# Kernel tuning notes

Measured on AMD Instinct MI355X. Metric: run time of the kernel, lower is better.

The kernel has to match this reference:

```python
import jax, jax.numpy as jnp
import numpy as np

ALPHA = 0.2  # LeakyReLU negative slope
OUT_FEATURES = 64

def setup_inputs() -> dict:
    key = jax.random.key(0)
    k1, k2, k3 = jax.random.split(key, 3)
    B, N, F_in, F_out = 16, 2048, 64, OUT_FEATURES
    h = jax.random.normal(k1, (B, N, F_in), dtype=jnp.float32)
    W = jax.random.normal(k2, (F_in, F_out), dtype=jnp.float32) * (1.414 / np.sqrt(F_in))
    a = jax.random.normal(k3, (2 * F_out, 1), dtype=jnp.float32) * 1.414
    return {"h": h, "W": W, "a": a}

def reference(h, W, a):
    F_out = W.shape[1]
    Wh = jnp.matmul(h, W)                        # [B, N, F_out]
    Wh1 = jnp.matmul(Wh, a[:F_out, :])           # [B, N, 1]
    Wh2 = jnp.matmul(Wh, a[F_out:, :])           # [B, N, 1]
    e = Wh1 + jnp.transpose(Wh2, (0, 2, 1))      # [B, N, N] broadcast add
    e = jnp.where(e >= 0, e, ALPHA * e)          # LeakyReLU
    attention = jax.nn.softmax(jax.nn.sigmoid(e), axis=1)  # softmax over dim=1 (faithful to source)
    h_prime = jnp.matmul(attention, Wh)          # [B, N, F_out]
    return jax.nn.elu(h_prime)                   # concat=True -> ELU
```

## Files before the change

### kernel.cpp

```cpp
#include <hip/hip_runtime.h>
#include <hip/hip_bf16.h>
#include <math.h>

#define NB 16
#define NN 2048
#define NF 64
#define LOG2E 1.44269504f

#define NT 4096
#define T_LO (-40.0f)
#define T_HI (10.0f)
#define T_SCALE (NT / (T_HI - T_LO))
#define Z_BIAS (-T_LO * T_SCALE)
#define Z_MAX ((float)(NT - 1))

#define MG 512
#define XG_LO (-96.0f)
#define DXG 0.375f
#define INV_DXG (1.0f / DXG)
#define U_BIAS (-XG_LO * INV_DXG)
#define U_MAX 510.999f

typedef __attribute__((ext_vector_type(8))) __bf16 bf16x8;
typedef __attribute__((ext_vector_type(8))) short  short8;
typedef __attribute__((ext_vector_type(4))) float  f32x4;

__device__ __forceinline__ float gexact(float t) {
    float v = t >= 0.f ? t : 0.2f * t;
    float s = 1.f / (1.f + expf(-v));
    return expf(s);
}

__device__ __forceinline__ float tlookup(const float* __restrict__ stab, float z) {
    float zc = __builtin_amdgcn_fmed3f(z, 0.f, Z_MAX);
    return stab[(int)zc];
}

__device__ __forceinline__ float elu(float v) {
    return v > 0.f ? v : (__builtin_amdgcn_exp2f(v * LOG2E) - 1.f);
}

__global__ __launch_bounds__(256) void k_prep(const float* __restrict__ h,
                                              const float* __restrict__ W,
                                              const float* __restrict__ a,
                                              uint4* __restrict__ vfrag,
                                              float* __restrict__ xs,
                                              float* __restrict__ ys,
                                              float* __restrict__ xs_u,
                                              float* __restrict__ ys_u,
                                              float* __restrict__ gtab) {
    __shared__ __attribute__((aligned(16))) float  hT[64 * 68];
    __shared__ __attribute__((aligned(16))) __bf16 WbT[64 * 72];
    __shared__ __attribute__((aligned(16))) __bf16 vT[64 * 74];
    __shared__ float uv[128];
    int t  = threadIdx.x;
    int r0 = blockIdx.x * 64;
    int b  = blockIdx.x >> 5;
    const float4* hsrc = (const float4*)(h + r0 * 64);
#pragma unroll
    for (int i = 0; i < 4; i++) {
        int flat = t + i * 256;
        int row = flat >> 4, c4 = flat & 15;
        float4 hv = hsrc[flat];
        float* dst = &hT[row * 68 + c4 * 4];
        dst[0] = hv.x; dst[1] = hv.y; dst[2] = hv.z; dst[3] = hv.w;
    }
#pragma unroll
    for (int i = 0; i < 4; i++) {
        int flat = t + i * 256;
        int k = flat >> 4, c4 = flat & 15;
        float4 wv = ((const float4*)W)[flat];
        WbT[(c4 * 4 + 0) * 72 + k] = (__bf16)wv.x;
        WbT[(c4 * 4 + 1) * 72 + k] = (__bf16)wv.y;
        WbT[(c4 * 4 + 2) * 72 + k] = (__bf16)wv.z;
        WbT[(c4 * 4 + 3) * 72 + k] = (__bf16)wv.w;
    }
    if (t < 64) {
        float s = 0.f;
#pragma unroll 8
        for (int f = 0; f < 64; f++) s = fmaf(W[t * 64 + f], a[f], s);
        uv[t] = s;
    } else if (t < 128) {
        int k = t - 64;
        float s = 0.f;
#pragma unroll 8
        for (int f = 0; f < 64; f++) s = fmaf(W[k * 64 + f], a[64 + f], s);
        uv[64 + k] = s;
    }
    __syncthreads();
    {
        int row = t >> 2, q = t & 3;
        const float* hp = &hT[row * 68 + q * 16];
        const float* up = &uv[q * 16];
        const float* vp = &uv[64 + q * 16];
        float sx = 0.f, sy = 0.f;
#pragma unroll
        for (int k2 = 0; k2 < 16; k2++) {
            float hv = hp[k2];
            sx = fmaf(hv, up[k2], sx);
            sy = fmaf(hv, vp[k2], sy);
        }
        sx += __shfl_xor(sx, 1); sx += __shfl_xor(sx, 2);
        sy += __shfl_xor(sy, 1); sy += __shfl_xor(sy, 2);
        if (q == 0) {
            int r = r0 + row;
            xs[r]   = T_SCALE * sx;
            ys[r]   = T_SCALE * sy;
            xs_u[r] = __builtin_amdgcn_fmed3f(sx * INV_DXG + U_BIAS, 0.f, U_MAX);
            ys_u[r] = __builtin_amdgcn_fmed3f(sy * INV_DXG + U_BIAS, 0.f, U_MAX);
        }
    }
    int w = t >> 6, lane = t & 63;
    int il = lane & 15, kg = lane >> 4;
    f32x4 acc0 = {0.f,0.f,0.f,0.f}, acc1 = {0.f,0.f,0.f,0.f};
    f32x4 acc2 = {0.f,0.f,0.f,0.f}, acc3 = {0.f,0.f,0.f,0.f};
#pragma unroll
    for (int ks = 0; ks < 2; ks++) {
        const float* ap = &hT[(w * 16 + il) * 68 + ks * 32 + kg * 8];
        bf16x8 af;
#pragma unroll
        for (int e = 0; e < 8; e++) af[e] = (__bf16)ap[e];
        bf16x8 b0 = *(const bf16x8*)&WbT[(0 * 16 + il) * 72 + ks * 32 + kg * 8];
        bf16x8 b1 = *(const bf16x8*)&WbT[(1 * 16 + il) * 72 + ks * 32 + kg * 8];
        bf16x8 b2 = *(const bf16x8*)&WbT[(2 * 16 + il) * 72 + ks * 32 + kg * 8];
        bf16x8 b3 = *(const bf16x8*)&WbT[(3 * 16 + il) * 72 + ks * 32 + kg * 8];
        acc0 = __builtin_amdgcn_mfma_f32_16x16x32_bf16(af, b0, acc0, 0, 0, 0);
        acc1 = __builtin_amdgcn_mfma_f32_16x16x32_bf16(af, b1, acc1, 0, 0, 0);
        acc2 = __builtin_amdgcn_mfma_f32_16x16x32_bf16(af, b2, acc2, 0, 0, 0);
        acc3 = __builtin_amdgcn_mfma_f32_16x16x32_bf16(af, b3, acc3, 0, 0, 0);
    }
#pragma unroll
    for (int r = 0; r < 4; r++) {
        __bf16* vrow = &vT[(w * 16 + kg * 4 + r) * 74 + il];
        vrow[0]  = (__bf16)acc0[r];
        vrow[16] = (__bf16)acc1[r];
        vrow[32] = (__bf16)acc2[r];
        vrow[48] = (__bf16)acc3[r];
    }
    __syncthreads();
#pragma unroll
    for (int s = 0; s < 2; s++) {
        int oi    = t + s * 256;
        int lane2 = oi & 63;
        int nt2   = (oi >> 6) & 3;
        int ksl   = oi >> 8;
        int rbase = ksl * 32 + ((lane2 >> 4) << 3);
        int col   = nt2 * 16 + (lane2 & 15);
        short8 o;
#pragma unroll
        for (int e = 0; e < 8; e++)
            o[e] = __builtin_bit_cast(short, vT[(rbase + e) * 74 + col]);
        int ks_g = ((blockIdx.x & 31) << 1) | ksl;
        vfrag[((b * 64 + ks_g) * 4 + nt2) * 64 + lane2] = __builtin_bit_cast(uint4, o);
    }
    if (blockIdx.x < 16) {
        int i = blockIdx.x * 256 + t;
        gtab[i] = gexact(T_LO + ((float)i + 0.5f) / T_SCALE);
    }
}

__global__ __launch_bounds__(256) void k_fbuild(const float* __restrict__ xs,
                                                const float* __restrict__ gtab,
                                                float* __restrict__ F) {
    __shared__ float stab[NT];
    __shared__ float xsb[NN];
    int tid = threadIdx.x;
    {
        const float4* src = (const float4*)gtab;
        float4*       dst = (float4*)stab;
#pragma unroll
        for (int k = 0; k < NT / 4 / 256; k++) dst[tid + k * 256] = src[tid + k * 256];
    }
    int mg = blockIdx.x & 127;
    int b  = blockIdx.x >> 7;
    {
        const float4* src = (const float4*)(xs + b * NN);
        float4*       dst = (float4*)xsb;
#pragma unroll
        for (int k = 0; k < NN / 4 / 256; k++) dst[tid + k * 256] = src[tid + k * 256];
    }
    __syncthreads();
    int w = tid >> 6, lane = tid & 63;
    int m = mg * 4 + w;
    float ymb = (XG_LO + (float)m * DXG) * T_SCALE + Z_BIAS;
    float acc = 0.f;
#pragma unroll 8
    for (int i8 = 0; i8 < NN / 64; i8++)
        acc += tlookup(stab, xsb[i8 * 64 + lane] + ymb);
#pragma unroll
    for (int s = 32; s; s >>= 1) acc += __shfl_xor(acc, s, 64);
    if (lane == 0) F[b * MG + m] = acc;
}

__global__ __launch_bounds__(512) void k_gbuild(const float* __restrict__ ys,
                                                const float* __restrict__ ys_u,
                                                const float* __restrict__ F,
                                                const float* __restrict__ gtab,
                                                const uint4* __restrict__ vfrag,
                                                float* __restrict__ G) {
    __shared__ float stab[NT];
    __shared__ float dinvb[NN];
    __shared__ float red[7][16][65];
    {
        const float4* src = (const float4*)gtab;
        float4*       dst = (float4*)stab;
#pragma unroll
        for (int k = 0; k < NT / 4 / 512; k++) dst[threadIdx.x + k * 512] = src[threadIdx.x + k * 512];
    }
    int b  = blockIdx.x >> 5;
    int ib = blockIdx.x & 31;
    {
        const float* Fb = F + b * MG;
#pragma unroll
        for (int i = 0; i < 4; i++) {
            int j = threadIdx.x + i * 512;
            float u  = ys_u[b * NN + j];
            int   k  = (int)u;
            float fr = u - (float)k;
            float d  = fmaf(Fb[k + 1] - Fb[k], fr, Fb[k]);
            dinvb[j] = __builtin_amdgcn_rcpf(d);
        }
    }
    int kz = threadIdx.x >> 6, lane = threadIdx.x & 63;
    int il = lane & 15, kg = lane >> 4;
    int mbase = ib * 16;

    float xgb = (XG_LO + (float)(mbase + il) * DXG) * T_SCALE + Z_BIAS;
    const float* ysb = ys + b * NN;
    const uint4* vfb = vfrag + b * 16384 + lane;
    __syncthreads();

    f32x4 acc0 = {0.f,0.f,0.f,0.f}, acc1 = {0.f,0.f,0.f,0.f};
    f32x4 acc2 = {0.f,0.f,0.f,0.f}, acc3 = {0.f,0.f,0.f,0.f};

    for (int ks = kz * 8; ks < kz * 8 + 8; ks++) {
        const float* yp = ysb + ks * 32 + kg * 8;
        const float* dp = &dinvb[ks * 32 + kg * 8];
        float4 ya = *reinterpret_cast<const float4*>(yp);
        float4 yb = *reinterpret_cast<const float4*>(yp + 4);
        float wv[8];
        wv[0] = tlookup(stab, xgb + ya.x);
        wv[1] = tlookup(stab, xgb + ya.y);
        wv[2] = tlookup(stab, xgb + ya.z);
        wv[3] = tlookup(stab, xgb + ya.w);
        wv[4] = tlookup(stab, xgb + yb.x);
        wv[5] = tlookup(stab, xgb + yb.y);
        wv[6] = tlookup(stab, xgb + yb.z);
        wv[7] = tlookup(stab, xgb + yb.w);
        bf16x8 af;
#pragma unroll
        for (int e = 0; e < 8; e++) af[e] = (__bf16)(wv[e] * dp[e]);

        const uint4* vp = vfb + ks * 256;
        bf16x8 b0 = __builtin_bit_cast(bf16x8, vp[0]);
        bf16x8 b1 = __builtin_bit_cast(bf16x8, vp[64]);
        bf16x8 b2 = __builtin_bit_cast(bf16x8, vp[128]);
        bf16x8 b3 = __builtin_bit_cast(bf16x8, vp[192]);

        acc0 = __builtin_amdgcn_mfma_f32_16x16x32_bf16(af, b0, acc0, 0, 0, 0);
        acc1 = __builtin_amdgcn_mfma_f32_16x16x32_bf16(af, b1, acc1, 0, 0, 0);
        acc2 = __builtin_amdgcn_mfma_f32_16x16x32_bf16(af, b2, acc2, 0, 0, 0);
        acc3 = __builtin_amdgcn_mfma_f32_16x16x32_bf16(af, b3, acc3, 0, 0, 0);
    }

    if (kz > 0) {
#pragma unroll
        for (int r = 0; r < 4; r++) {
            float* rp = &red[kz - 1][kg * 4 + r][il];
            rp[0]  = acc0[r];
            rp[16] = acc1[r];
            rp[32] = acc2[r];
            rp[48] = acc3[r];
        }
    }
    __syncthreads();
    if (kz == 0) {
        int gbase = (b * MG + mbase + kg * 4) * 64 + il;
#pragma unroll
        for (int r = 0; r < 4; r++) {
            float s0 = acc0[r], s1 = acc1[r], s2 = acc2[r], s3 = acc3[r];
#pragma unroll
            for (int p = 0; p < 7; p++) {
                const float* rp = &red[p][kg * 4 + r][il];
                s0 += rp[0]; s1 += rp[16]; s2 += rp[32]; s3 += rp[48];
            }
            float* grow = G + gbase + r * 64;
            grow[0] = s0; grow[16] = s1; grow[32] = s2; grow[48] = s3;
        }
    }
}

__global__ __launch_bounds__(256) void k_apply(const float* __restrict__ xs_u,
                                               const float* __restrict__ G,
                                               float* __restrict__ out) {
    int w = threadIdx.x >> 6, f = threadIdx.x & 63;
    int r = blockIdx.x * 4 + w;
    int b = r >> 11;
    float u  = xs_u[r];
    int   k  = (int)u;
    float fr = u - (float)k;
    const float* Gb = G + (b * MG + k) * 64;
    float g0 = Gb[f];
    float g1 = Gb[64 + f];
    out[r * 64 + f] = elu(fmaf(g1 - g0, fr, g0));
}

extern "C" void kernel_launch(void* const* d_in, const int* in_sizes, int n_in,
                              void* d_out, int out_size, void* d_ws, size_t ws_size,
                              hipStream_t stream) {
    const float* h = (const float*)d_in[0];
    const float* W = (const float*)d_in[1];
    const float* a = (const float*)d_in[2];
    float* out = (float*)d_out;

    float*  xs    = (float*)d_ws;
    float*  ys    = xs + NB * NN;
    float*  xs_u  = ys + NB * NN;
    float*  ys_u  = xs_u + NB * NN;
    float*  F     = ys_u + NB * NN;
    float*  G     = F + NB * MG;
    uint4*  vfrag = (uint4*)(G + NB * MG * NF);
    float*  gtab  = (float*)(vfrag + NB * NN * NF / 8);

    k_prep<<<dim3(NB * NN / 64), dim3(256), 0, stream>>>(h, W, a, vfrag, xs, ys, xs_u, ys_u, gtab);
    k_fbuild<<<dim3(NB * (MG / 4)), dim3(256), 0, stream>>>(xs, gtab, F);
    k_gbuild<<<dim3(NB * (MG / 16)), dim3(512), 0, stream>>>(ys, ys_u, F, gtab, vfrag, G);
    k_apply<<<dim3(NB * NN / 4), dim3(256), 0, stream>>>(xs_u, G, out);
}
```

Measured before the change: 37.54 us.

## Replace F-build kernel with histogram convolution fused into G-build

Removes the separate k_fbuild launch, which did a table lookup for every x per grid point. Inside k_gbuild, each block now builds a linearly interpolated histogram of the batch's x values over the grid using LDS atomics. It then convolves that histogram with a precomputed 1D g table written by k_prep to get the column sums F. This cuts one launch and the O(N·M) lookups, but every gbuild block redundantly recomputes F (512x512 FMAs plus atomics) and adds interpolation error from binning x.

```diff
diff --git a/kernel.cpp b/kernel.cpp
--- a/kernel.cpp
+++ b/kernel.cpp
@@ -20,6 +20,7 @@
 #define INV_DXG (1.0f / DXG)
 #define U_BIAS (-XG_LO * INV_DXG)
 #define U_MAX 510.999f
+#define GS_N 1024
 
 typedef __attribute__((ext_vector_type(8))) __bf16 bf16x8;
 typedef __attribute__((ext_vector_type(8))) short  short8;
@@ -44,11 +45,11 @@
                                               const float* __restrict__ W,
                                               const float* __restrict__ a,
                                               uint4* __restrict__ vfrag,
-                                              float* __restrict__ xs,
                                               float* __restrict__ ys,
                                               float* __restrict__ xs_u,
                                               float* __restrict__ ys_u,
-                                              float* __restrict__ gtab) {
+                                              float* __restrict__ gtab,
+                                              float* __restrict__ gs) {
     __shared__ __attribute__((aligned(16))) float  hT[64 * 68];
     __shared__ __attribute__((aligned(16))) __bf16 WbT[64 * 72];
     __shared__ __attribute__((aligned(16))) __bf16 vT[64 * 74];
@@ -104,7 +105,6 @@
         sy += __shfl_xor(sy, 1); sy += __shfl_xor(sy, 2);
         if (q == 0) {
             int r = r0 + row;
-            xs[r]   = T_SCALE * sx;
             ys[r]   = T_SCALE * sy;
             xs_u[r] = __builtin_amdgcn_fmed3f(sx * INV_DXG + U_BIAS, 0.f, U_MAX);
             ys_u[r] = __builtin_amdgcn_fmed3f(sy * INV_DXG + U_BIAS, 0.f, U_MAX);
@@ -156,72 +156,62 @@
     if (blockIdx.x < 16) {
         int i = blockIdx.x * 256 + t;
         gtab[i] = gexact(T_LO + ((float)i + 0.5f) / T_SCALE);
-    }
-}
-
-__global__ __launch_bounds__(256) void k_fbuild(const float* __restrict__ xs,
-                                                const float* __restrict__ gtab,
-                                                float* __restrict__ F) {
-    __shared__ float stab[NT];
-    __shared__ float xsb[NN];
-    int tid = threadIdx.x;
-    {
-        const float4* src = (const float4*)gtab;
-        float4*       dst = (float4*)stab;
-#pragma unroll
-        for (int k = 0; k < NT / 4 / 256; k++) dst[tid + k * 256] = src[tid + k * 256];
-    }
-    int mg = blockIdx.x & 127;
-    int b  = blockIdx.x >> 7;
-    {
-        const float4* src = (const float4*)(xs + b * NN);
-        float4*       dst = (float4*)xsb;
-#pragma unroll
-        for (int k = 0; k < NN / 4 / 256; k++) dst[tid + k * 256] = src[tid + k * 256];
-    }
-    __syncthreads();
-    int w = tid >> 6, lane = tid & 63;
-    int m = mg * 4 + w;
-    float ymb = (XG_LO + (float)m * DXG) * T_SCALE + Z_BIAS;
-    float acc = 0.f;
-#pragma unroll 8
-    for (int i8 = 0; i8 < NN / 64; i8++)
-        acc += tlookup(stab, xsb[i8 * 64 + lane] + ymb);
-#pragma unroll
-    for (int s = 32; s; s >>= 1) acc += __shfl_xor(acc, s, 64);
-    if (lane == 0) F[b * MG + m] = acc;
+    } else if (blockIdx.x < 20) {
+        int i = (blockIdx.x - 16) * 256 + t;
+        gs[i] = gexact(2.f * XG_LO + (float)i * DXG);
+    }
 }
 
 __global__ __launch_bounds__(512) void k_gbuild(const float* __restrict__ ys,
                                                 const float* __restrict__ ys_u,
-                                                const float* __restrict__ F,
+                                                const float* __restrict__ xs_u,
                                                 const float* __restrict__ gtab,
+                                                const float* __restrict__ gs,
                                                 const uint4* __restrict__ vfrag,
                                                 float* __restrict__ G) {
     __shared__ float stab[NT];
     __shared__ float dinvb[NN];
     __shared__ float red[7][16][65];
+    float* gsb = &red[0][0][0];
+    float* hxb = gsb + GS_N;
+    float* Fb  = hxb + MG;
+    int t = threadIdx.x;
+    int b  = blockIdx.x >> 5;
+    int ib = blockIdx.x & 31;
     {
         const float4* src = (const float4*)gtab;
         float4*       dst = (float4*)stab;
 #pragma unroll
-        for (int k = 0; k < NT / 4 / 512; k++) dst[threadIdx.x + k * 512] = src[threadIdx.x + k * 512];
-    }
-    int b  = blockIdx.x >> 5;
-    int ib = blockIdx.x & 31;
+        for (int k = 0; k < NT / 4 / 512; k++) dst[t + k * 512] = src[t + k * 512];
+    }
+    if (t < 256) ((float4*)gsb)[t] = ((const float4*)gs)[t];
+    hxb[t] = 0.f;
+    __syncthreads();
+#pragma unroll
+    for (int i = 0; i < 4; i++) {
+        float xu = xs_u[b * NN + i * 512 + t];
+        int   k  = (int)xu;
+        float fr = xu - (float)k;
+        atomicAdd(&hxb[k],     1.f - fr);
+        atomicAdd(&hxb[k + 1], fr);
+    }
+    __syncthreads();
     {
-        const float* Fb = F + b * MG;
-#pragma unroll
-        for (int i = 0; i < 4; i++) {
-            int j = threadIdx.x + i * 512;
-            float u  = ys_u[b * NN + j];
-            int   k  = (int)u;
-            float fr = u - (float)k;
-            float d  = fmaf(Fb[k + 1] - Fb[k], fr, Fb[k]);
-            dinvb[j] = __builtin_amdgcn_rcpf(d);
-        }
-    }
-    int kz = threadIdx.x >> 6, lane = threadIdx.x & 63;
+        float acc = 0.f;
+        for (int k = 0; k < MG; k++) acc = fmaf(hxb[k], gsb[k + t], acc);
+        Fb[t] = acc;
+    }
+    __syncthreads();
+#pragma unroll
+    for (int i = 0; i < 4; i++) {
+        int j = t + i * 512;
+        float u  = ys_u[b * NN + j];
+        int   k  = (int)u;
+        float fr = u - (float)k;
+        float d  = fmaf(Fb[k + 1] - Fb[k], fr, Fb[k]);
+        dinvb[j] = __builtin_amdgcn_rcpf(d);
+    }
+    int kz = t >> 6, lane = t & 63;
     int il = lane & 15, kg = lane >> 4;
     int mbase = ib * 16;
 
@@ -313,17 +303,15 @@
     const float* a = (const float*)d_in[2];
     float* out = (float*)d_out;
 
-    float*  xs    = (float*)d_ws;
-    float*  ys    = xs + NB * NN;
+    float*  ys    = (float*)d_ws;
     float*  xs_u  = ys + NB * NN;
     float*  ys_u  = xs_u + NB * NN;
-    float*  F     = ys_u + NB * NN;
-    float*  G     = F + NB * MG;
+    float*  G     = ys_u + NB * NN;
     uint4*  vfrag = (uint4*)(G + NB * MG * NF);
     float*  gtab  = (float*)(vfrag + NB * NN * NF / 8);
-
-    k_prep<<<dim3(NB * NN / 64), dim3(256), 0, stream>>>(h, W, a, vfrag, xs, ys, xs_u, ys_u, gtab);
-    k_fbuild<<<dim3(NB * (MG / 4)), dim3(256), 0, stream>>>(xs, gtab, F);
-    k_gbuild<<<dim3(NB * (MG / 16)), dim3(512), 0, stream>>>(ys, ys_u, F, gtab, vfrag, G);
+    float*  gs    = gtab + NT;
+
+    k_prep<<<dim3(NB * NN / 64), dim3(256), 0, stream>>>(h, W, a, vfrag, ys, xs_u, ys_u, gtab, gs);
+    k_gbuild<<<dim3(NB * (MG / 16)), dim3(512), 0, stream>>>(ys, ys_u, xs_u, gtab, gs, vfrag, G);
     k_apply<<<dim3(NB * NN / 4), dim3(256), 0, stream>>>(xs_u, G, out);
 }
```

New measurement: 50.54 us. 1.35x slower.

## Fuse F-table build into prep kernel using grid-sampled g and atomics

Applied to the files above, without the earlier changes.

Drops the separate k_fbuild kernel. Each k_prep block now builds a small shared table of the exact g function on the DXG grid and uses its rows' grid-interpolated xs coordinates to add into F with atomicAdd. F is zeroed with a memset beforehand. This removes one kernel launch and the xs round trip through memory, but it changes the approximation: F is now built from interpolated grid values instead of the fine lookup table. It also adds per-block exp work, shared-memory reads and global atomics.

```diff
diff --git a/kernel.cpp b/kernel.cpp
--- a/kernel.cpp
+++ b/kernel.cpp
@@ -20,6 +20,7 @@
 #define INV_DXG (1.0f / DXG)
 #define U_BIAS (-XG_LO * INV_DXG)
 #define U_MAX 510.999f
+#define GS_N 1024
 
 typedef __attribute__((ext_vector_type(8))) __bf16 bf16x8;
 typedef __attribute__((ext_vector_type(8))) short  short8;
@@ -44,18 +45,24 @@
                                               const float* __restrict__ W,
                                               const float* __restrict__ a,
                                               uint4* __restrict__ vfrag,
-                                              float* __restrict__ xs,
                                               float* __restrict__ ys,
                                               float* __restrict__ xs_u,
                                               float* __restrict__ ys_u,
+                                              float* __restrict__ F,
                                               float* __restrict__ gtab) {
     __shared__ __attribute__((aligned(16))) float  hT[64 * 68];
     __shared__ __attribute__((aligned(16))) __bf16 WbT[64 * 72];
     __shared__ __attribute__((aligned(16))) __bf16 vT[64 * 74];
     __shared__ float uv[128];
+    __shared__ float gsb[GS_N];
+    __shared__ int   kuA[64];
+    __shared__ float frA[64];
     int t  = threadIdx.x;
     int r0 = blockIdx.x * 64;
     int b  = blockIdx.x >> 5;
+#pragma unroll
+    for (int i = t; i < GS_N; i += 256)
+        gsb[i] = gexact(2.f * XG_LO + (float)i * DXG);
     const float4* hsrc = (const float4*)(h + r0 * 64);
 #pragma unroll
     for (int i = 0; i < 4; i++) {
@@ -104,10 +111,13 @@
         sy += __shfl_xor(sy, 1); sy += __shfl_xor(sy, 2);
         if (q == 0) {
             int r = r0 + row;
-            xs[r]   = T_SCALE * sx;
+            float xu = __builtin_amdgcn_fmed3f(sx * INV_DXG + U_BIAS, 0.f, U_MAX);
             ys[r]   = T_SCALE * sy;
-            xs_u[r] = __builtin_amdgcn_fmed3f(sx * INV_DXG + U_BIAS, 0.f, U_MAX);
+            xs_u[r] = xu;
             ys_u[r] = __builtin_amdgcn_fmed3f(sy * INV_DXG + U_BIAS, 0.f, U_MAX);
+            int ku  = (int)xu;
+            kuA[row] = ku;
+            frA[row] = xu - (float)ku;
         }
     }
     int w = t >> 6, lane = t & 63;
@@ -153,43 +163,25 @@
         int ks_g = ((blockIdx.x & 31) << 1) | ksl;
         vfrag[((b * 64 + ks_g) * 4 + nt2) * 64 + lane2] = __builtin_bit_cast(uint4, o);
     }
+    {
+        float a0 = 0.f, a1 = 0.f;
+#pragma unroll 8
+        for (int r = 0; r < 64; r++) {
+            int   ku = kuA[r];
+            float fr = frA[r];
+            float w0 = 1.f - fr;
+            const float* g0 = &gsb[ku + t];
+            const float* g1 = &gsb[ku + t + 256];
+            a0 = fmaf(w0, g0[0], a0); a0 = fmaf(fr, g0[1], a0);
+            a1 = fmaf(w0, g1[0], a1); a1 = fmaf(fr, g1[1], a1);
+        }
+        atomicAdd(&F[b * MG + t], a0);
+        atomicAdd(&F[b * MG + t + 256], a1);
+    }
     if (blockIdx.x < 16) {
         int i = blockIdx.x * 256 + t;
         gtab[i] = gexact(T_LO + ((float)i + 0.5f) / T_SCALE);
     }
-}
-
-__global__ __launch_bounds__(256) void k_fbuild(const float* __restrict__ xs,
-                                                const float* __restrict__ gtab,
-                                                float* __restrict__ F) {
-    __shared__ float stab[NT];
-    __shared__ float xsb[NN];
-    int tid = threadIdx.x;
-    {
-        const float4* src = (const float4*)gtab;
-        float4*       dst = (float4*)stab;
-#pragma unroll
-        for (int k = 0; k < NT / 4 / 256; k++) dst[tid + k * 256] = src[tid + k * 256];
-    }
-    int mg = blockIdx.x & 127;
-    int b  = blockIdx.x >> 7;
-    {
-        const float4* src = (const float4*)(xs + b * NN);
-        float4*       dst = (float4*)xsb;
-#pragma unroll
-        for (int k = 0; k < NN / 4 / 256; k++) dst[tid + k * 256] = src[tid + k * 256];
-    }
-    __syncthreads();
-    int w = tid >> 6, lane = tid & 63;
-    int m = mg * 4 + w;
-    float ymb = (XG_LO + (float)m * DXG) * T_SCALE + Z_BIAS;
-    float acc = 0.f;
-#pragma unroll 8
-    for (int i8 = 0; i8 < NN / 64; i8++)
-        acc += tlookup(stab, xsb[i8 * 64 + lane] + ymb);
-#pragma unroll
-    for (int s = 32; s; s >>= 1) acc += __shfl_xor(acc, s, 64);
-    if (lane == 0) F[b * MG + m] = acc;
 }
 
 __global__ __launch_bounds__(512) void k_gbuild(const float* __restrict__ ys,
@@ -313,8 +305,7 @@
     const float* a = (const float*)d_in[2];
     float* out = (float*)d_out;
 
-    float*  xs    = (float*)d_ws;
-    float*  ys    = xs + NB * NN;
+    float*  ys    = (float*)d_ws;
     float*  xs_u  = ys + NB * NN;
     float*  ys_u  = xs_u + NB * NN;
     float*  F     = ys_u + NB * NN;
@@ -322,8 +313,8 @@
     uint4*  vfrag = (uint4*)(G + NB * MG * NF);
     float*  gtab  = (float*)(vfrag + NB * NN * NF / 8);
 
-    k_prep<<<dim3(NB * NN / 64), dim3(256), 0, stream>>>(h, W, a, vfrag, xs, ys, xs_u, ys_u, gtab);
-    k_fbuild<<<dim3(NB * (MG / 4)), dim3(256), 0, stream>>>(xs, gtab, F);
+    hipMemsetAsync(F, 0, NB * MG * sizeof(float), stream);
+    k_prep<<<dim3(NB * NN / 64), dim3(256), 0, stream>>>(h, W, a, vfrag, ys, xs_u, ys_u, F, gtab);
     k_gbuild<<<dim3(NB * (MG / 16)), dim3(512), 0, stream>>>(ys, ys_u, F, gtab, vfrag, G);
     k_apply<<<dim3(NB * NN / 4), dim3(256), 0, stream>>>(xs_u, G, out);
 }
```

New measurement: 39.98 us. +6.5%, slower.
